# Optimization experiments

Measured on AMD Instinct MI355X. Metric: run time of the kernel, lower is better.

Reference implementation:

```python
import jax, jax.numpy as jnp
import numpy as np

EPS = 1e-8
LAM = 0.7  # resonance_lambda


def phase_resonance(a, b, eps=EPS):
    # a, b: (B, N, D) float32. Pairwise phase coherence -> (B, N, N)
    D = a.shape[-1]
    pairs = (D // 2)
    a2 = a[..., :pairs * 2].reshape(*a.shape[:-1], pairs, 2)
    b2 = b[..., :pairs * 2].reshape(*b.shape[:-1], pairs, 2)
    theta_a = jnp.arctan2(a2[..., 1] + eps, a2[..., 0] + eps)  # (B,N,pairs)
    theta_b = jnp.arctan2(b2[..., 1] + eps, b2[..., 0] + eps)  # (B,N,pairs)
    delta = theta_a[:, :, None, :] - theta_b[:, None, :, :]    # (B,N,N,pairs)
    return jnp.cos(delta).mean(axis=-1)                        # (B,N,N)


def setup_inputs() -> dict:
    key = jax.random.key(0)
    k1, k2, k3, k4, k5 = jax.random.split(key, 5)
    B, N, D = 2, 1024, 128
    node_states = jax.random.normal(k1, (B, N, D), dtype=jnp.float32)
    node_gates = jax.random.uniform(k2, (B, N, 1), dtype=jnp.float32)
    r_acc = jax.random.normal(k3, (B, N, N), dtype=jnp.float32)
    # nn.Linear(D, D, bias=False) weights, y = x @ W.T
    scale = 1.0 / np.sqrt(D)
    W_in = jax.random.uniform(k4, (D, D), dtype=jnp.float32, minval=-scale, maxval=scale)
    W_out = jax.random.uniform(k5, (D, D), dtype=jnp.float32, minval=-scale, maxval=scale)
    conductance = jnp.asarray(1.0, dtype=jnp.float32)
    return {"node_states": node_states, "node_gates": node_gates, "r_acc": r_acc,
            "W_in": W_in, "W_out": W_out, "conductance": conductance}


def reference(node_states, node_gates, r_acc, W_in, W_out, conductance):
    B, N, D = node_states.shape
    h = node_states @ W_in.T                                   # field_in projection
    r_instant = phase_resonance(h, h)                          # (B,N,N)
    r_acc_new = LAM * r_acc + (1.0 - LAM) * r_instant
    r_acc_new = jnp.clip(r_acc_new, -2.0, 2.0)
    cond = jnp.clip(conductance, -5.0, 5.0)
    coupling = jax.nn.sigmoid(cond * r_acc_new)                # (B,N,N)
    eye = jnp.eye(N, dtype=coupling.dtype)[None]               # zero self-coupling
    coupling = coupling * (1.0 - eye)
    coupling = coupling * jnp.swapaxes(node_gates, -1, -2)     # (B,1,N) col gates
    coupling = coupling * node_gates                           # (B,N,1) row gates
    coupling = coupling / (coupling.sum(axis=-1, keepdims=True) + 1e-8)
    transmitted = node_states * node_gates
    values = transmitted @ W_out.T                             # field_out projection
    field_signal = coupling @ values                           # (B,N,D)
    return field_signal, r_acc_new
```

## Files before the change

### kernel.cpp

```cpp
#include <hip/hip_runtime.h>
#include <hip/hip_bf16.h>

using bf16x8 = __attribute__((ext_vector_type(8))) short;
using f32x4  = __attribute__((ext_vector_type(4))) float;

#define NN 1024
#define DD 128

__device__ __forceinline__ short bf16b(float f) {
    __hip_bfloat16 t = __float2bfloat16(f);
    return *(short*)&t;
}

__device__ __forceinline__ bf16x8 cvt8(const float* __restrict__ p) {
    float4 a = *(const float4*)p;
    float4 b = *(const float4*)(p + 4);
    bf16x8 r;
    r[0] = bf16b(a.x); r[1] = bf16b(a.y); r[2] = bf16b(a.z); r[3] = bf16b(a.w);
    r[4] = bf16b(b.x); r[5] = bf16b(b.y); r[6] = bf16b(b.z); r[7] = bf16b(b.w);
    return r;
}

__global__ __launch_bounds__(256) void prep_kernel(
    const float* __restrict__ states, const float* __restrict__ gates,
    const float* __restrict__ W_in, const float* __restrict__ W_out,
    __hip_bfloat16* __restrict__ M_bf, __hip_bfloat16* __restrict__ valT)
{
    __shared__ __align__(16) short s_m[16][136];
    __shared__ __align__(16) short s_vT[128][24];

    const int tid = threadIdx.x;
    const int l = tid & 63, w = tid >> 6;
    const int row_a = l & 15, kg = l >> 4;
    const int b  = blockIdx.x >> 6;
    const int n0 = (blockIdx.x & 63) * 16;
    const int colbase = w * 32;

    const float* A = states + ((size_t)b * NN + n0) * DD;

    f32x4 accH[2], accV[2];
    #pragma unroll
    for (int cp = 0; cp < 2; ++cp) {
        accH[cp] = (f32x4){0.f, 0.f, 0.f, 0.f};
        accV[cp] = (f32x4){0.f, 0.f, 0.f, 0.f};
    }

    #pragma unroll
    for (int ks = 0; ks < 4; ++ks) {
        int koff = (ks * 4 + kg) * 8;
        bf16x8 a = cvt8(A + row_a * DD + koff);
        #pragma unroll
        for (int cp = 0; cp < 2; ++cp) {
            int d = colbase + cp * 16 + row_a;
            bf16x8 b1 = cvt8(W_in  + d * DD + koff);
            bf16x8 b2 = cvt8(W_out + d * DD + koff);
            accH[cp] = __builtin_amdgcn_mfma_f32_16x16x32_bf16(a, b1, accH[cp], 0, 0, 0);
            accV[cp] = __builtin_amdgcn_mfma_f32_16x16x32_bf16(a, b2, accV[cp], 0, 0, 0);
        }
    }

    float g[4];
    #pragma unroll
    for (int q = 0; q < 4; ++q) g[q] = gates[b * NN + n0 + kg * 4 + q];

    const bool odd = (row_a & 1) != 0;
    #pragma unroll
    for (int cp = 0; cp < 2; ++cp) {
        #pragma unroll
        for (int q = 0; q < 4; ++q) {
            float hm = accH[cp][q] + 1e-8f;
            float hp = __shfl_xor(hm, 1);
            float x = odd ? hp : hm;
            float y = odd ? hm : hp;
            float r2 = x * x + y * y;
            float out;
            if (r2 > 0.f) out = (odd ? y : x) * rsqrtf(r2);
            else          out = odd ? 0.f : 1.f;
            s_m[kg * 4 + q][colbase + cp * 16 + row_a] = bf16b(out);
            s_vT[colbase + cp * 16 + row_a][kg * 4 + q] = bf16b(accV[cp][q] * g[q]);
        }
    }
    __syncthreads();

    {
        int r = tid >> 4, seg = tid & 15;
        bf16x8 v = *(const bf16x8*)&s_m[r][seg * 8];
        *(bf16x8*)(M_bf + ((size_t)b * NN + n0 + r) * DD + seg * 8) = v;
    }
    {
        int d = tid >> 1, half = tid & 1;
        bf16x8 v = *(const bf16x8*)&s_vT[d][half * 8];
        *(bf16x8*)(valT + ((size_t)b * DD + d) * NN + n0 + half * 8) = v;
    }
}

__global__ __launch_bounds__(256) void fused_kernel(
    const __hip_bfloat16* __restrict__ M_bf,
    const __hip_bfloat16* __restrict__ valT,
    const float* __restrict__ r_acc,
    const float* __restrict__ gates,
    const float* __restrict__ cond_ptr,
    float* __restrict__ r_out,
    __hip_bfloat16* __restrict__ part,
    float* __restrict__ part_rs)
{
    __shared__ __align__(16) short s_cpl[16][136];
    __shared__ float s_rs[16][4];

    const int tid = threadIdx.x;
    const int l = tid & 63, w = tid >> 6;
    const int row_a = l & 15, kg = l >> 4;
    const int jq = blockIdx.x;
    const int j0 = jq * 128;
    const int i0 = blockIdx.y * 16;
    const int b  = blockIdx.z;

    const bf16x8* Mv = (const bf16x8*)(M_bf + (size_t)b * NN * DD);
    const bf16x8* Vv = (const bf16x8*)(valT + (size_t)b * DD * NN);

    f32x4 acc[2];
    acc[0] = (f32x4){0.f, 0.f, 0.f, 0.f};
    acc[1] = (f32x4){0.f, 0.f, 0.f, 0.f};
    #pragma unroll
    for (int ks = 0; ks < 4; ++ks) {
        bf16x8 a = Mv[(size_t)(i0 + row_a) * 16 + ks * 4 + kg];
        #pragma unroll
        for (int cp = 0; cp < 2; ++cp) {
            bf16x8 bb = Mv[(size_t)(j0 + w * 32 + cp * 16 + row_a) * 16 + ks * 4 + kg];
            acc[cp] = __builtin_amdgcn_mfma_f32_16x16x32_bf16(a, bb, acc[cp], 0, 0, 0);
        }
    }

    const float cond = fminf(fmaxf(cond_ptr[0], -5.f), 5.f);
    float g_i[4], g_j[2];
    #pragma unroll
    for (int q = 0; q < 4; ++q) g_i[q] = gates[(size_t)b * NN + i0 + kg * 4 + q];
    #pragma unroll
    for (int cp = 0; cp < 2; ++cp) g_j[cp] = gates[(size_t)b * NN + j0 + w * 32 + cp * 16 + row_a];

    const size_t robase = (size_t)b * NN * NN;
    float rs[4] = {0.f, 0.f, 0.f, 0.f};

    #pragma unroll
    for (int q = 0; q < 4; ++q) {
        const int i = i0 + kg * 4 + q;
        const float gi = g_i[q];
        #pragma unroll
        for (int cp = 0; cp < 2; ++cp) {
            const int jl = w * 32 + cp * 16 + row_a;
            const int j  = j0 + jl;
            float s  = acc[cp][q] * (1.f / 64.f);
            float ra = r_acc[robase + (size_t)i * NN + j];
            float rn = fminf(fmaxf(0.7f * ra + 0.3f * s, -2.f), 2.f);
            r_out[robase + (size_t)i * NN + j] = rn;
            float cpl = (i == j) ? 0.f
                        : (1.f / (1.f + __expf(-cond * rn))) * gi * g_j[cp];
            rs[q] += cpl;
            s_cpl[kg * 4 + q][jl] = bf16b(cpl);
        }
    }

    #pragma unroll
    for (int q = 0; q < 4; ++q) {
        float v = rs[q];
        v += __shfl_xor(v, 1);
        v += __shfl_xor(v, 2);
        v += __shfl_xor(v, 4);
        v += __shfl_xor(v, 8);
        if (row_a == 0) s_rs[kg * 4 + q][w] = v;
    }
    __syncthreads();

    f32x4 pacc[2];
    pacc[0] = (f32x4){0.f, 0.f, 0.f, 0.f};
    pacc[1] = (f32x4){0.f, 0.f, 0.f, 0.f};
    #pragma unroll
    for (int ks2 = 0; ks2 < 4; ++ks2) {
        bf16x8 a = *(const bf16x8*)&s_cpl[row_a][(ks2 * 4 + kg) * 8];
        #pragma unroll
        for (int dt = 0; dt < 2; ++dt) {
            int d = w * 32 + dt * 16 + row_a;
            bf16x8 bb = Vv[(size_t)d * (NN / 8) + (j0 >> 3) + ks2 * 4 + kg];
            pacc[dt] = __builtin_amdgcn_mfma_f32_16x16x32_bf16(a, bb, pacc[dt], 0, 0, 0);
        }
    }

    __hip_bfloat16* pb = part + ((size_t)jq * 2 + b) * NN * DD;
    #pragma unroll
    for (int dt = 0; dt < 2; ++dt) {
        #pragma unroll
        for (int q = 0; q < 4; ++q) {
            int i = i0 + kg * 4 + q;
            int d = w * 32 + dt * 16 + row_a;
            pb[(size_t)i * DD + d] = __float2bfloat16(pacc[dt][q]);
        }
    }

    if (tid < 16)
        part_rs[((size_t)jq * 2 + b) * NN + i0 + tid] =
            s_rs[tid][0] + s_rs[tid][1] + s_rs[tid][2] + s_rs[tid][3];
}

__global__ __launch_bounds__(256) void reduce_kernel(
    const __hip_bfloat16* __restrict__ part,
    const float* __restrict__ part_rs,
    float* __restrict__ field)
{
    int t   = blockIdx.x * 256 + threadIdx.x;
    int b   = t >> 15;
    int rem = t & 32767;
    int i   = rem >> 5;
    int d4  = (rem & 31) * 4;
    size_t ibase = (size_t)i * DD + d4;

    float s0 = 0.f, s1 = 0.f, s2 = 0.f, s3 = 0.f, rsum = 0.f;
    #pragma unroll
    for (int jq = 0; jq < 8; ++jq) {
        size_t slab = ((size_t)jq * 2 + b);
        uint2 u = *(const uint2*)(part + slab * NN * DD + ibase);
        s0 += __uint_as_float(u.x << 16);
        s1 += __uint_as_float(u.x & 0xffff0000u);
        s2 += __uint_as_float(u.y << 16);
        s3 += __uint_as_float(u.y & 0xffff0000u);
        rsum += part_rs[slab * NN + i];
    }
    float inv = 1.0f / (rsum + 1e-8f);
    float4 o = {s0 * inv, s1 * inv, s2 * inv, s3 * inv};
    *(float4*)(field + ((size_t)b * NN + i) * DD + d4) = o;
}

extern "C" void kernel_launch(void* const* d_in, const int* in_sizes, int n_in,
                              void* d_out, int out_size, void* d_ws, size_t ws_size,
                              hipStream_t stream) {
    const float* states = (const float*)d_in[0];
    const float* gates  = (const float*)d_in[1];
    const float* r_acc  = (const float*)d_in[2];
    const float* W_in   = (const float*)d_in[3];
    const float* W_out  = (const float*)d_in[4];
    const float* cond   = (const float*)d_in[5];

    float* field = (float*)d_out;
    float* r_out = field + 2 * NN * DD;

    char* ws = (char*)d_ws;
    __hip_bfloat16* M_bf    = (__hip_bfloat16*)ws;
    __hip_bfloat16* valT    = (__hip_bfloat16*)(ws + (512 << 10));
    __hip_bfloat16* part    = (__hip_bfloat16*)(ws + (1 << 20));
    float*          part_rs = (float*)(ws + (5 << 20));

    hipLaunchKernelGGL(prep_kernel, dim3(128), dim3(256), 0, stream,
                       states, gates, W_in, W_out, M_bf, valT);
    hipLaunchKernelGGL(fused_kernel, dim3(8, 64, 2), dim3(256), 0, stream,
                       M_bf, valT, r_acc, gates, cond, r_out, part, part_rs);
    hipLaunchKernelGGL(reduce_kernel, dim3(256), dim3(256), 0, stream,
                       part, part_rs, field);
}
```

Measured before the change: 97.73 us.

## Stage resonance tile through LDS for vectorized r_acc I/O and halve j-tile

The fused kernel now writes the MFMA resonance accumulators into an LDS tile and re-reads them row-major, so each thread loads r_acc and stores r_out as contiguous float4 pairs instead of scattered scalar accesses. The j tile shrinks from 128 to 64 columns with 128-thread blocks, doubling the grid. The second MFMA is rebalanced to 4 d-tiles per wave, and row sums go straight to global. The cost is twice as many bf16 partial slabs for the reduce kernel to read and write, plus an extra LDS round trip and barrier.

```diff
diff --git a/kernel.cpp b/kernel.cpp
--- a/kernel.cpp
+++ b/kernel.cpp
@@ -94,7 +94,7 @@
     }
 }
 
-__global__ __launch_bounds__(256) void fused_kernel(
+__global__ __launch_bounds__(128) void fused_kernel(
     const __hip_bfloat16* __restrict__ M_bf,
     const __hip_bfloat16* __restrict__ valT,
     const float* __restrict__ r_acc,
@@ -104,14 +104,14 @@
     __hip_bfloat16* __restrict__ part,
     float* __restrict__ part_rs)
 {
-    __shared__ __align__(16) short s_cpl[16][136];
-    __shared__ float s_rs[16][4];
+    __shared__ float s_S[16][65];
+    __shared__ __align__(16) short s_cpl[16][72];
 
     const int tid = threadIdx.x;
     const int l = tid & 63, w = tid >> 6;
     const int row_a = l & 15, kg = l >> 4;
     const int jq = blockIdx.x;
-    const int j0 = jq * 128;
+    const int j0 = jq * 64;
     const int i0 = blockIdx.y * 16;
     const int b  = blockIdx.z;
 
@@ -131,55 +131,68 @@
         }
     }
 
+    #pragma unroll
+    for (int q = 0; q < 4; ++q) {
+        #pragma unroll
+        for (int cp = 0; cp < 2; ++cp)
+            s_S[kg * 4 + q][w * 32 + cp * 16 + row_a] = acc[cp][q];
+    }
+    __syncthreads();
+
+    const int row = tid >> 3;
+    const int j8  = (tid & 7) * 8;
+    const int i   = i0 + row;
     const float cond = fminf(fmaxf(cond_ptr[0], -5.f), 5.f);
-    float g_i[4], g_j[2];
-    #pragma unroll
-    for (int q = 0; q < 4; ++q) g_i[q] = gates[(size_t)b * NN + i0 + kg * 4 + q];
-    #pragma unroll
-    for (int cp = 0; cp < 2; ++cp) g_j[cp] = gates[(size_t)b * NN + j0 + w * 32 + cp * 16 + row_a];
-
-    const size_t robase = (size_t)b * NN * NN;
-    float rs[4] = {0.f, 0.f, 0.f, 0.f};
-
-    #pragma unroll
-    for (int q = 0; q < 4; ++q) {
-        const int i = i0 + kg * 4 + q;
-        const float gi = g_i[q];
-        #pragma unroll
-        for (int cp = 0; cp < 2; ++cp) {
-            const int jl = w * 32 + cp * 16 + row_a;
-            const int j  = j0 + jl;
-            float s  = acc[cp][q] * (1.f / 64.f);
-            float ra = r_acc[robase + (size_t)i * NN + j];
-            float rn = fminf(fmaxf(0.7f * ra + 0.3f * s, -2.f), 2.f);
-            r_out[robase + (size_t)i * NN + j] = rn;
-            float cpl = (i == j) ? 0.f
-                        : (1.f / (1.f + __expf(-cond * rn))) * gi * g_j[cp];
-            rs[q] += cpl;
-            s_cpl[kg * 4 + q][jl] = bf16b(cpl);
-        }
-    }
-
-    #pragma unroll
-    for (int q = 0; q < 4; ++q) {
-        float v = rs[q];
-        v += __shfl_xor(v, 1);
-        v += __shfl_xor(v, 2);
-        v += __shfl_xor(v, 4);
-        v += __shfl_xor(v, 8);
-        if (row_a == 0) s_rs[kg * 4 + q][w] = v;
-    }
+    const float gi = gates[(size_t)b * NN + i];
+    const float* gjp = gates + (size_t)b * NN + j0 + j8;
+    float4 gj0 = *(const float4*)gjp;
+    float4 gj1 = *(const float4*)(gjp + 4);
+    float gj[8] = {gj0.x, gj0.y, gj0.z, gj0.w, gj1.x, gj1.y, gj1.z, gj1.w};
+
+    const size_t off = (size_t)b * NN * NN + (size_t)i * NN + j0 + j8;
+    float4 ra0 = *(const float4*)(r_acc + off);
+    float4 ra1 = *(const float4*)(r_acc + off + 4);
+    float ra[8] = {ra0.x, ra0.y, ra0.z, ra0.w, ra1.x, ra1.y, ra1.z, ra1.w};
+
+    float rn[8], cpl[8];
+    float rs = 0.f;
+    #pragma unroll
+    for (int jj = 0; jj < 8; ++jj) {
+        float s = s_S[row][j8 + jj] * (1.f / 64.f);
+        float r = fminf(fmaxf(0.7f * ra[jj] + 0.3f * s, -2.f), 2.f);
+        rn[jj] = r;
+        float c = (i == j0 + j8 + jj) ? 0.f
+                  : (1.f / (1.f + __expf(-cond * r))) * gi * gj[jj];
+        cpl[jj] = c;
+        rs += c;
+    }
+    *(float4*)(r_out + off)     = (float4){rn[0], rn[1], rn[2], rn[3]};
+    *(float4*)(r_out + off + 4) = (float4){rn[4], rn[5], rn[6], rn[7]};
+
+    {
+        bf16x8 pk;
+        #pragma unroll
+        for (int jj = 0; jj < 8; ++jj) pk[jj] = bf16b(cpl[jj]);
+        *(bf16x8*)&s_cpl[row][j8] = pk;
+    }
+
+    rs += __shfl_xor(rs, 1);
+    rs += __shfl_xor(rs, 2);
+    rs += __shfl_xor(rs, 4);
+    if ((tid & 7) == 0)
+        part_rs[((size_t)jq * 2 + b) * NN + i] = rs;
     __syncthreads();
 
-    f32x4 pacc[2];
-    pacc[0] = (f32x4){0.f, 0.f, 0.f, 0.f};
-    pacc[1] = (f32x4){0.f, 0.f, 0.f, 0.f};
-    #pragma unroll
-    for (int ks2 = 0; ks2 < 4; ++ks2) {
+    f32x4 pacc[4];
+    #pragma unroll
+    for (int dt = 0; dt < 4; ++dt) pacc[dt] = (f32x4){0.f, 0.f, 0.f, 0.f};
+
+    #pragma unroll
+    for (int ks2 = 0; ks2 < 2; ++ks2) {
         bf16x8 a = *(const bf16x8*)&s_cpl[row_a][(ks2 * 4 + kg) * 8];
         #pragma unroll
-        for (int dt = 0; dt < 2; ++dt) {
-            int d = w * 32 + dt * 16 + row_a;
+        for (int dt = 0; dt < 4; ++dt) {
+            int d = w * 64 + dt * 16 + row_a;
             bf16x8 bb = Vv[(size_t)d * (NN / 8) + (j0 >> 3) + ks2 * 4 + kg];
             pacc[dt] = __builtin_amdgcn_mfma_f32_16x16x32_bf16(a, bb, pacc[dt], 0, 0, 0);
         }
@@ -187,18 +200,14 @@
 
     __hip_bfloat16* pb = part + ((size_t)jq * 2 + b) * NN * DD;
     #pragma unroll
-    for (int dt = 0; dt < 2; ++dt) {
+    for (int dt = 0; dt < 4; ++dt) {
         #pragma unroll
         for (int q = 0; q < 4; ++q) {
-            int i = i0 + kg * 4 + q;
-            int d = w * 32 + dt * 16 + row_a;
-            pb[(size_t)i * DD + d] = __float2bfloat16(pacc[dt][q]);
-        }
-    }
-
-    if (tid < 16)
-        part_rs[((size_t)jq * 2 + b) * NN + i0 + tid] =
-            s_rs[tid][0] + s_rs[tid][1] + s_rs[tid][2] + s_rs[tid][3];
+            int ii = i0 + kg * 4 + q;
+            int d  = w * 64 + dt * 16 + row_a;
+            pb[(size_t)ii * DD + d] = __float2bfloat16(pacc[dt][q]);
+        }
+    }
 }
 
 __global__ __launch_bounds__(256) void reduce_kernel(
@@ -215,7 +224,7 @@
 
     float s0 = 0.f, s1 = 0.f, s2 = 0.f, s3 = 0.f, rsum = 0.f;
     #pragma unroll
-    for (int jq = 0; jq < 8; ++jq) {
+    for (int jq = 0; jq < 16; ++jq) {
         size_t slab = ((size_t)jq * 2 + b);
         uint2 u = *(const uint2*)(part + slab * NN * DD + ibase);
         s0 += __uint_as_float(u.x << 16);
@@ -246,11 +255,11 @@
     __hip_bfloat16* M_bf    = (__hip_bfloat16*)ws;
     __hip_bfloat16* valT    = (__hip_bfloat16*)(ws + (512 << 10));
     __hip_bfloat16* part    = (__hip_bfloat16*)(ws + (1 << 20));
-    float*          part_rs = (float*)(ws + (5 << 20));
+    float*          part_rs = (float*)(ws + (9 << 20));
 
     hipLaunchKernelGGL(prep_kernel, dim3(128), dim3(256), 0, stream,
                        states, gates, W_in, W_out, M_bf, valT);
-    hipLaunchKernelGGL(fused_kernel, dim3(8, 64, 2), dim3(256), 0, stream,
+    hipLaunchKernelGGL(fused_kernel, dim3(16, 64, 2), dim3(128), 0, stream,
                        M_bf, valT, r_acc, gates, cond, r_out, part, part_rs);
     hipLaunchKernelGGL(reduce_kernel, dim3(256), dim3(256), 0, stream,
                        part, part_rs, field);
```

Measured after the change: 99.48 us. About the same (+1.8%).
